# Kernel optimization log

Measured on AMD Instinct MI355X. Metric: run time of the kernel, lower is better.

Reference implementation:

```python
import jax, jax.numpy as jnp
import numpy as np

LN_EPS = 1e-5

def _ln(x, g, b):
    m = x.mean(-1, keepdims=True)
    v = jnp.mean((x - m) ** 2, axis=-1, keepdims=True)
    return (x - m) * jax.lax.rsqrt(v + LN_EPS) * g + b


def setup_inputs() -> dict:
    key = jax.random.key(0)
    ks = jax.random.split(key, 8)
    B, S, H = 8, 4096, 2048
    V, L, E = 32, 8, 64   # vocab_size, symbol seq_len, embedding_dim
    sc = 0.02
    d = {}
    d["hidden_states"] = jax.random.normal(ks[0], (B, S, H), jnp.float32)
    # uniform in (0,1) for Gumbel noise: g = -log(-log(u))
    d["gumbel_u"] = jax.random.uniform(ks[1], (B, L, V), jnp.float32, 1e-6, 1.0 - 1e-6)
    d["enc_w1"] = jax.random.normal(ks[2], (256, H), jnp.float32) * sc
    d["enc_b1"] = jnp.zeros((256,), jnp.float32)
    d["ln1_g"] = jnp.ones((256,), jnp.float32)
    d["ln1_b"] = jnp.zeros((256,), jnp.float32)
    d["enc_w2"] = jax.random.normal(ks[3], (L * V, 256), jnp.float32) * sc
    d["enc_b2"] = jnp.zeros((L * V,), jnp.float32)
    d["embed"] = jax.random.normal(ks[4], (V, E), jnp.float32) * sc
    d["dec_w1"] = jax.random.normal(ks[5], (256, L * E), jnp.float32) * sc
    d["dec_b1"] = jnp.zeros((256,), jnp.float32)
    d["ln2_g"] = jnp.ones((256,), jnp.float32)
    d["ln2_b"] = jnp.zeros((256,), jnp.float32)
    d["dec_w2"] = jax.random.normal(ks[6], (H, 256), jnp.float32) * sc
    d["dec_b2"] = jnp.zeros((H,), jnp.float32)
    return d


def reference(hidden_states, gumbel_u, enc_w1, enc_b1, ln1_g, ln1_b, enc_w2, enc_b2,
              embed, dec_w1, dec_b1, ln2_g, ln2_b, dec_w2, dec_b2):
    V, L, TAU = 32, 8, 1.0
    B, S, H = hidden_states.shape
    E = embed.shape[1]
    # encode: mean-pool over sequence, then MLP -> logits [B, L, V]
    pooled = hidden_states.mean(axis=1)
    h = _ln(pooled @ enc_w1.T + enc_b1, ln1_g, ln1_b)
    h = jax.nn.gelu(h, approximate=False)
    logits = (h @ enc_w2.T + enc_b2).reshape(B, L, V)
    # gumbel-softmax with straight-through (hard) estimator
    g = -jnp.log(-jnp.log(gumbel_u))
    y_soft = jax.nn.softmax((logits + g) / TAU, axis=-1)
    idx = jnp.argmax(y_soft, axis=-1)
    y_hard = jax.nn.one_hot(idx, V, dtype=y_soft.dtype)
    soft_symbols = y_hard - jax.lax.stop_gradient(y_soft) + y_soft
    # decode: embed symbols, flatten, MLP back to hidden size
    emb = jnp.einsum('blv,ve->ble', soft_symbols, embed).reshape(B, L * E)
    dh = _ln(emb @ dec_w1.T + dec_b1, ln2_g, ln2_b)
    dh = jax.nn.gelu(dh, approximate=False)
    decoded = dh @ dec_w2.T + dec_b2            # [B, H]
    # residual + 0.1 * broadcast over sequence
    return hidden_states + 0.1 * decoded[:, None, :]
```

## Files before the change

kernel.cpp:

```cpp
#include <hip/hip_runtime.h>
#include <math.h>

#define B 8
#define S 4096
#define H 2048
#define LSYM 8
#define EMB 64
#define SPLIT 128
#define CHUNK (S / SPLIT)

__global__ __launch_bounds__(256) void pool_partial(const float* __restrict__ hid,
                                                    float* __restrict__ part) {
    const int sp = blockIdx.x;
    const int b  = blockIdx.y;
    const int t  = threadIdx.x;
    const float* slab = hid + (size_t)b * S * H + (size_t)sp * CHUNK * H;
    const int iters = CHUNK * (H / 1024);
    float4 a0 = {0.f, 0.f, 0.f, 0.f};
    float4 a1 = {0.f, 0.f, 0.f, 0.f};
    float4 a2 = {0.f, 0.f, 0.f, 0.f};
    float4 a3 = {0.f, 0.f, 0.f, 0.f};
#pragma unroll 4
    for (int i = 0; i < iters; i += 4) {
        const float4 v0 = *reinterpret_cast<const float4*>(slab + (size_t)i * 1024 + t * 4);
        const float4 v1 = *reinterpret_cast<const float4*>(slab + (size_t)(i + 1) * 1024 + t * 4);
        const float4 v2 = *reinterpret_cast<const float4*>(slab + (size_t)(i + 2) * 1024 + t * 4);
        const float4 v3 = *reinterpret_cast<const float4*>(slab + (size_t)(i + 3) * 1024 + t * 4);
        a0.x += v0.x; a0.y += v0.y; a0.z += v0.z; a0.w += v0.w;
        a1.x += v1.x; a1.y += v1.y; a1.z += v1.z; a1.w += v1.w;
        a2.x += v2.x; a2.y += v2.y; a2.z += v2.z; a2.w += v2.w;
        a3.x += v3.x; a3.y += v3.y; a3.z += v3.z; a3.w += v3.w;
    }
    float4 e, o;
    e.x = a0.x + a2.x; e.y = a0.y + a2.y; e.z = a0.z + a2.z; e.w = a0.w + a2.w;
    o.x = a1.x + a3.x; o.y = a1.y + a3.y; o.z = a1.z + a3.z; o.w = a1.w + a3.w;
    float* dst = part + ((size_t)sp * B + b) * H;
    *reinterpret_cast<float4*>(dst + t * 4)        = e;
    *reinterpret_cast<float4*>(dst + 1024 + t * 4) = o;
}

__global__ __launch_bounds__(256) void pool_reduce(const float* __restrict__ part,
                                                   float* __restrict__ pooled) {
    const int i4 = blockIdx.x * 256 + threadIdx.x;
    if (i4 >= B * H / 4) return;
    float4 acc = {0.f, 0.f, 0.f, 0.f};
    for (int sp = 0; sp < SPLIT; ++sp) {
        const float4 v = *reinterpret_cast<const float4*>(part + (size_t)sp * B * H + (size_t)i4 * 4);
        acc.x += v.x; acc.y += v.y; acc.z += v.z; acc.w += v.w;
    }
    const float inv = 1.0f / (float)S;
    acc.x *= inv; acc.y *= inv; acc.z *= inv; acc.w *= inv;
    *reinterpret_cast<float4*>(pooled + (size_t)i4 * 4) = acc;
}

__global__ __launch_bounds__(256) void enc1_matvec(const float* __restrict__ pooled,
                                                   const float* __restrict__ ew1,
                                                   const float* __restrict__ eb1,
                                                   float* __restrict__ out1) {
    const int wv   = (blockIdx.x * 256 + threadIdx.x) >> 6;
    const int lane = threadIdx.x & 63;
    const int b = wv >> 8, t = wv & 255;
    const float4* wrow = reinterpret_cast<const float4*>(ew1 + (size_t)t * H);
    const float4* prow = reinterpret_cast<const float4*>(pooled + b * H);
    float acc = 0.f;
#pragma unroll
    for (int i = 0; i < 8; ++i) {
        const float4 w = wrow[lane + 64 * i];
        const float4 p = prow[lane + 64 * i];
        acc += w.x * p.x + w.y * p.y + w.z * p.z + w.w * p.w;
    }
    for (int off = 32; off; off >>= 1) acc += __shfl_xor(acc, off, 64);
    if (lane == 0) out1[b * 256 + t] = acc + eb1[t];
}

__device__ __forceinline__ float block_sum256(float x, float* red) {
    const int t = threadIdx.x;
    red[t] = x;
    __syncthreads();
    for (int s = 128; s > 0; s >>= 1) {
        if (t < s) red[t] += red[t + s];
        __syncthreads();
    }
    const float r = red[0];
    __syncthreads();
    return r;
}

__global__ __launch_bounds__(256) void mlp_middle(
    const float* __restrict__ out1, const float* __restrict__ gu,
    const float* __restrict__ g1,  const float* __restrict__ bb1,
    const float* __restrict__ ew2, const float* __restrict__ eb2,
    const float* __restrict__ emb_tab,
    const float* __restrict__ dw1, const float* __restrict__ db1,
    const float* __restrict__ g2,  const float* __restrict__ bb2,
    float* __restrict__ hs2) {
    __shared__ float red[256];
    __shared__ float hs[256];
    __shared__ float es[LSYM * EMB];

    const int b = blockIdx.x;
    const int t = threadIdx.x;

    float acc = out1[b * 256 + t];
    {
        const float m = block_sum256(acc, red) * (1.0f / 256.0f);
        const float d = acc - m;
        const float v = block_sum256(d * d, red) * (1.0f / 256.0f);
        float x = d * rsqrtf(v + 1e-5f) * g1[t] + bb1[t];
        x = 0.5f * x * (1.0f + erff(x * 0.70710678118654752f));
        hs[t] = x;
    }
    __syncthreads();

    float z;
    {
        float a2 = eb2[t];
        const float* w2row = ew2 + t * 256;
        for (int k = 0; k < 256; k += 4) {
            const float4 w = *reinterpret_cast<const float4*>(w2row + k);
            a2 += w.x * hs[k] + w.y * hs[k + 1] + w.z * hs[k + 2] + w.w * hs[k + 3];
        }
        const float u = gu[b * 256 + t];
        z = a2 - logf(-logf(u));
    }

    {
        int   bi = t & 31;
        float bz = z;
        for (int off = 16; off; off >>= 1) {
            const float oz = __shfl_xor(bz, off, 32);
            const int   oi = __shfl_xor(bi, off, 32);
            if (oz > bz || (oz == bz && oi < bi)) { bz = oz; bi = oi; }
        }
        const int l = t >> 5, v32 = t & 31;
        es[l * EMB + v32]      = emb_tab[bi * EMB + v32];
        es[l * EMB + 32 + v32] = emb_tab[bi * EMB + 32 + v32];
    }
    __syncthreads();

    float a3 = db1[t];
    {
        const float* d1row = dw1 + t * (LSYM * EMB);
        for (int k = 0; k < LSYM * EMB; k += 4) {
            const float4 w = *reinterpret_cast<const float4*>(d1row + k);
            a3 += w.x * es[k] + w.y * es[k + 1] + w.z * es[k + 2] + w.w * es[k + 3];
        }
    }
    {
        const float m2 = block_sum256(a3, red) * (1.0f / 256.0f);
        const float dd = a3 - m2;
        const float vv = block_sum256(dd * dd, red) * (1.0f / 256.0f);
        float y = dd * rsqrtf(vv + 1e-5f) * g2[t] + bb2[t];
        y = 0.5f * y * (1.0f + erff(y * 0.70710678118654752f));
        hs2[b * 256 + t] = y;
    }
}

__global__ __launch_bounds__(256) void dec2_matvec(const float* __restrict__ hs2,
                                                   const float* __restrict__ dw2,
                                                   const float* __restrict__ db2,
                                                   float* __restrict__ dec_sc) {
    const int wv   = (blockIdx.x * 256 + threadIdx.x) >> 6;
    const int lane = threadIdx.x & 63;
    const int b = wv >> 11, j = wv & 2047;
    const float4 w = reinterpret_cast<const float4*>(dw2 + (size_t)j * 256)[lane];
    const float4 h = reinterpret_cast<const float4*>(hs2 + b * 256)[lane];
    float acc = w.x * h.x + w.y * h.y + w.z * h.z + w.w * h.w;
    for (int off = 32; off; off >>= 1) acc += __shfl_xor(acc, off, 64);
    if (lane == 0) dec_sc[b * 2048 + j] = 0.1f * (acc + db2[j]);
}

__global__ __launch_bounds__(256) void residual_add(const float* __restrict__ hid,
                                                    const float* __restrict__ dec,
                                                    float* __restrict__ out) {
    const size_t tid0 = (size_t)blockIdx.x * 256 + threadIdx.x;
    const int h4 = (int)(tid0 & (H / 4 - 1));
    const float4* __restrict__ hv4 = reinterpret_cast<const float4*>(hid);
    const float4* __restrict__ dv4 = reinterpret_cast<const float4*>(dec);
    float4* __restrict__ ov4 = reinterpret_cast<float4*>(out);
    size_t i = tid0;
#pragma unroll
    for (int b = 0; b < B; ++b) {
        const float4 dv = dv4[b * (H / 4) + h4];
#pragma unroll
        for (int r = 0; r < 4; ++r, i += (size_t)1 << 19) {
            const float4 hv = hv4[i];
            float4 o;
            o.x = hv.x + dv.x; o.y = hv.y + dv.y; o.z = hv.z + dv.z; o.w = hv.w + dv.w;
            ov4[i] = o;
        }
    }
}

extern "C" void kernel_launch(void* const* d_in, const int* in_sizes, int n_in,
                              void* d_out, int out_size, void* d_ws, size_t ws_size,
                              hipStream_t stream) {
    const float* hid   = (const float*)d_in[0];
    const float* gu    = (const float*)d_in[1];
    const float* ew1   = (const float*)d_in[2];
    const float* eb1   = (const float*)d_in[3];
    const float* g1    = (const float*)d_in[4];
    const float* bb1   = (const float*)d_in[5];
    const float* ew2   = (const float*)d_in[6];
    const float* eb2   = (const float*)d_in[7];
    const float* emb   = (const float*)d_in[8];
    const float* dw1   = (const float*)d_in[9];
    const float* db1   = (const float*)d_in[10];
    const float* g2    = (const float*)d_in[11];
    const float* bb2   = (const float*)d_in[12];
    const float* dw2   = (const float*)d_in[13];
    const float* db2   = (const float*)d_in[14];
    float* out = (float*)d_out;

    float* part   = (float*)d_ws;
    float* pooled = part + (size_t)SPLIT * B * H;
    float* dec_sc = pooled + (size_t)B * H;
    float* out1   = dec_sc + (size_t)B * H;
    float* hs2    = out1 + (size_t)B * 256;

    pool_partial<<<dim3(SPLIT, B), 256, 0, stream>>>(hid, part);
    pool_reduce<<<(B * H / 4 + 255) / 256, 256, 0, stream>>>(part, pooled);
    enc1_matvec<<<B * 256 / 4, 256, 0, stream>>>(pooled, ew1, eb1, out1);
    mlp_middle<<<B, 256, 0, stream>>>(out1, gu, g1, bb1, ew2, eb2, emb,
                                      dw1, db1, g2, bb2, hs2);
    dec2_matvec<<<B * 2048 / 4, 256, 0, stream>>>(hs2, dw2, db2, dec_sc);
    residual_add<<<2048, 256, 0, stream>>>(hid, dec_sc, out);
}
```

Before: 211.3 us.

## Fuse pool reduce, encoder MLP, gumbel and decoder into one kernel

Merges pool_reduce, enc1_matvec, mlp_middle and dec2_matvec into a single 1024-thread kernel with 4 blocks per batch. Each block redundantly recomputes the pooled vector and encoder/decoder MLP, then computes one quarter of the dec_w2 outputs. It also halves SPLIT and widens the pool_partial unroll to 8 accumulators. This removes three launches and several global round-trips, but it runs the small-MLP stage on only 32 blocks and duplicates work across them, which may leave the serial middle section slower.

```diff
diff --git a/kernel.cpp b/kernel.cpp
--- a/kernel.cpp
+++ b/kernel.cpp
@@ -6,8 +6,9 @@
 #define H 2048
 #define LSYM 8
 #define EMB 64
-#define SPLIT 128
+#define SPLIT 64
 #define CHUNK (S / SPLIT)
+#define QPB 4
 
 __global__ __launch_bounds__(256) void pool_partial(const float* __restrict__ hid,
                                                     float* __restrict__ part) {
@@ -16,115 +17,111 @@
     const int t  = threadIdx.x;
     const float* slab = hid + (size_t)b * S * H + (size_t)sp * CHUNK * H;
     const int iters = CHUNK * (H / 1024);
-    float4 a0 = {0.f, 0.f, 0.f, 0.f};
-    float4 a1 = {0.f, 0.f, 0.f, 0.f};
-    float4 a2 = {0.f, 0.f, 0.f, 0.f};
-    float4 a3 = {0.f, 0.f, 0.f, 0.f};
-#pragma unroll 4
-    for (int i = 0; i < iters; i += 4) {
-        const float4 v0 = *reinterpret_cast<const float4*>(slab + (size_t)i * 1024 + t * 4);
-        const float4 v1 = *reinterpret_cast<const float4*>(slab + (size_t)(i + 1) * 1024 + t * 4);
-        const float4 v2 = *reinterpret_cast<const float4*>(slab + (size_t)(i + 2) * 1024 + t * 4);
-        const float4 v3 = *reinterpret_cast<const float4*>(slab + (size_t)(i + 3) * 1024 + t * 4);
-        a0.x += v0.x; a0.y += v0.y; a0.z += v0.z; a0.w += v0.w;
-        a1.x += v1.x; a1.y += v1.y; a1.z += v1.z; a1.w += v1.w;
-        a2.x += v2.x; a2.y += v2.y; a2.z += v2.z; a2.w += v2.w;
-        a3.x += v3.x; a3.y += v3.y; a3.z += v3.z; a3.w += v3.w;
+    float4 a[8];
+#pragma unroll
+    for (int k = 0; k < 8; ++k) a[k] = make_float4(0.f, 0.f, 0.f, 0.f);
+    for (int i = 0; i < iters; i += 8) {
+#pragma unroll
+        for (int k = 0; k < 8; ++k) {
+            const float4 v = *reinterpret_cast<const float4*>(slab + (size_t)(i + k) * 1024 + t * 4);
+            a[k].x += v.x; a[k].y += v.y; a[k].z += v.z; a[k].w += v.w;
+        }
     }
     float4 e, o;
-    e.x = a0.x + a2.x; e.y = a0.y + a2.y; e.z = a0.z + a2.z; e.w = a0.w + a2.w;
-    o.x = a1.x + a3.x; o.y = a1.y + a3.y; o.z = a1.z + a3.z; o.w = a1.w + a3.w;
+    e.x = a[0].x + a[2].x + a[4].x + a[6].x;  e.y = a[0].y + a[2].y + a[4].y + a[6].y;
+    e.z = a[0].z + a[2].z + a[4].z + a[6].z;  e.w = a[0].w + a[2].w + a[4].w + a[6].w;
+    o.x = a[1].x + a[3].x + a[5].x + a[7].x;  o.y = a[1].y + a[3].y + a[5].y + a[7].y;
+    o.z = a[1].z + a[3].z + a[5].z + a[7].z;  o.w = a[1].w + a[3].w + a[5].w + a[7].w;
     float* dst = part + ((size_t)sp * B + b) * H;
     *reinterpret_cast<float4*>(dst + t * 4)        = e;
     *reinterpret_cast<float4*>(dst + 1024 + t * 4) = o;
 }
 
-__global__ __launch_bounds__(256) void pool_reduce(const float* __restrict__ part,
-                                                   float* __restrict__ pooled) {
-    const int i4 = blockIdx.x * 256 + threadIdx.x;
-    if (i4 >= B * H / 4) return;
-    float4 acc = {0.f, 0.f, 0.f, 0.f};
-    for (int sp = 0; sp < SPLIT; ++sp) {
-        const float4 v = *reinterpret_cast<const float4*>(part + (size_t)sp * B * H + (size_t)i4 * 4);
-        acc.x += v.x; acc.y += v.y; acc.z += v.z; acc.w += v.w;
-    }
-    const float inv = 1.0f / (float)S;
-    acc.x *= inv; acc.y *= inv; acc.z *= inv; acc.w *= inv;
-    *reinterpret_cast<float4*>(pooled + (size_t)i4 * 4) = acc;
-}
-
-__global__ __launch_bounds__(256) void enc1_matvec(const float* __restrict__ pooled,
-                                                   const float* __restrict__ ew1,
-                                                   const float* __restrict__ eb1,
-                                                   float* __restrict__ out1) {
-    const int wv   = (blockIdx.x * 256 + threadIdx.x) >> 6;
-    const int lane = threadIdx.x & 63;
-    const int b = wv >> 8, t = wv & 255;
-    const float4* wrow = reinterpret_cast<const float4*>(ew1 + (size_t)t * H);
-    const float4* prow = reinterpret_cast<const float4*>(pooled + b * H);
-    float acc = 0.f;
-#pragma unroll
-    for (int i = 0; i < 8; ++i) {
-        const float4 w = wrow[lane + 64 * i];
-        const float4 p = prow[lane + 64 * i];
-        acc += w.x * p.x + w.y * p.y + w.z * p.z + w.w * p.w;
-    }
-    for (int off = 32; off; off >>= 1) acc += __shfl_xor(acc, off, 64);
-    if (lane == 0) out1[b * 256 + t] = acc + eb1[t];
-}
-
-__device__ __forceinline__ float block_sum256(float x, float* red) {
+__device__ __forceinline__ float block_sum1024(float x, float* red16) {
     const int t = threadIdx.x;
-    red[t] = x;
-    __syncthreads();
-    for (int s = 128; s > 0; s >>= 1) {
-        if (t < s) red[t] += red[t + s];
-        __syncthreads();
-    }
-    const float r = red[0];
+    const int lane = t & 63, wv = t >> 6;
+    for (int off = 32; off; off >>= 1) x += __shfl_xor(x, off, 64);
+    if (lane == 0) red16[wv] = x;
+    __syncthreads();
+    float r = 0.f;
+#pragma unroll
+    for (int i = 0; i < 16; ++i) r += red16[i];
     __syncthreads();
     return r;
 }
 
-__global__ __launch_bounds__(256) void mlp_middle(
-    const float* __restrict__ out1, const float* __restrict__ gu,
+__global__ __launch_bounds__(1024) void mega(
+    const float* __restrict__ part, const float* __restrict__ gu,
+    const float* __restrict__ ew1, const float* __restrict__ eb1,
     const float* __restrict__ g1,  const float* __restrict__ bb1,
     const float* __restrict__ ew2, const float* __restrict__ eb2,
     const float* __restrict__ emb_tab,
     const float* __restrict__ dw1, const float* __restrict__ db1,
     const float* __restrict__ g2,  const float* __restrict__ bb2,
-    float* __restrict__ hs2) {
-    __shared__ float red[256];
-    __shared__ float hs[256];
+    const float* __restrict__ dw2, const float* __restrict__ db2,
+    float* __restrict__ dec_sc) {
+    __shared__ float pooled[H];
+    __shared__ float red16[16];
+    __shared__ float out1s[256];
+    __shared__ float hsm[256];
     __shared__ float es[LSYM * EMB];
-
-    const int b = blockIdx.x;
+    __shared__ float hs2s[256];
+
+    const int blk = blockIdx.x;
+    const int b = blk >> 2, q = blk & (QPB - 1);
     const int t = threadIdx.x;
-
-    float acc = out1[b * 256 + t];
-    {
-        const float m = block_sum256(acc, red) * (1.0f / 256.0f);
-        const float d = acc - m;
-        const float v = block_sum256(d * d, red) * (1.0f / 256.0f);
-        float x = d * rsqrtf(v + 1e-5f) * g1[t] + bb1[t];
+    const int wv = t >> 6, lane = t & 63;
+
+    if (t < H / 4) {
+        const float4* pp = reinterpret_cast<const float4*>(part);
+        float4 acc = {0.f, 0.f, 0.f, 0.f};
+#pragma unroll 4
+        for (int sp = 0; sp < SPLIT; ++sp) {
+            const float4 v = pp[((size_t)sp * B + b) * (H / 4) + t];
+            acc.x += v.x; acc.y += v.y; acc.z += v.z; acc.w += v.w;
+        }
+        const float inv = 1.0f / (float)S;
+        acc.x *= inv; acc.y *= inv; acc.z *= inv; acc.w *= inv;
+        *reinterpret_cast<float4*>(&pooled[t * 4]) = acc;
+    }
+    __syncthreads();
+
+#pragma unroll
+    for (int k = 0; k < 16; ++k) {
+        const int tt = wv * 16 + k;
+        const float4* wrow = reinterpret_cast<const float4*>(ew1 + (size_t)tt * H);
+        float acc = 0.f;
+#pragma unroll
+        for (int i = 0; i < 8; ++i) {
+            const float4 w = wrow[lane + 64 * i];
+            const float4 p = *reinterpret_cast<const float4*>(&pooled[(lane + 64 * i) * 4]);
+            acc += w.x * p.x + w.y * p.y + w.z * p.z + w.w * p.w;
+        }
+        for (int off = 32; off; off >>= 1) acc += __shfl_xor(acc, off, 64);
+        if (lane == 0) out1s[tt] = acc + eb1[tt];
+    }
+    __syncthreads();
+
+    float x0 = (t < 256) ? out1s[t] : 0.f;
+    const float m1 = block_sum1024(x0, red16) * (1.0f / 256.0f);
+    const float d1 = (t < 256) ? (x0 - m1) : 0.f;
+    const float v1 = block_sum1024(d1 * d1, red16) * (1.0f / 256.0f);
+    if (t < 256) {
+        float x = d1 * rsqrtf(v1 + 1e-5f) * g1[t] + bb1[t];
         x = 0.5f * x * (1.0f + erff(x * 0.70710678118654752f));
-        hs[t] = x;
-    }
-    __syncthreads();
-
-    float z;
-    {
+        hsm[t] = x;
+    }
+    __syncthreads();
+
+    if (t < 256) {
         float a2 = eb2[t];
         const float* w2row = ew2 + t * 256;
         for (int k = 0; k < 256; k += 4) {
             const float4 w = *reinterpret_cast<const float4*>(w2row + k);
-            a2 += w.x * hs[k] + w.y * hs[k + 1] + w.z * hs[k + 2] + w.w * hs[k + 3];
+            a2 += w.x * hsm[k] + w.y * hsm[k + 1] + w.z * hsm[k + 2] + w.w * hsm[k + 3];
         }
         const float u = gu[b * 256 + t];
-        z = a2 - logf(-logf(u));
-    }
-
-    {
+        const float z = a2 - logf(-logf(u));
         int   bi = t & 31;
         float bz = z;
         for (int off = 16; off; off >>= 1) {
@@ -138,36 +135,34 @@
     }
     __syncthreads();
 
-    float a3 = db1[t];
-    {
+    float a3 = 0.f;
+    if (t < 256) {
+        a3 = db1[t];
         const float* d1row = dw1 + t * (LSYM * EMB);
         for (int k = 0; k < LSYM * EMB; k += 4) {
             const float4 w = *reinterpret_cast<const float4*>(d1row + k);
             a3 += w.x * es[k] + w.y * es[k + 1] + w.z * es[k + 2] + w.w * es[k + 3];
         }
     }
-    {
-        const float m2 = block_sum256(a3, red) * (1.0f / 256.0f);
-        const float dd = a3 - m2;
-        const float vv = block_sum256(dd * dd, red) * (1.0f / 256.0f);
-        float y = dd * rsqrtf(vv + 1e-5f) * g2[t] + bb2[t];
+    const float m2 = block_sum1024((t < 256) ? a3 : 0.f, red16) * (1.0f / 256.0f);
+    const float d2 = (t < 256) ? (a3 - m2) : 0.f;
+    const float v2 = block_sum1024(d2 * d2, red16) * (1.0f / 256.0f);
+    if (t < 256) {
+        float y = d2 * rsqrtf(v2 + 1e-5f) * g2[t] + bb2[t];
         y = 0.5f * y * (1.0f + erff(y * 0.70710678118654752f));
-        hs2[b * 256 + t] = y;
-    }
-}
-
-__global__ __launch_bounds__(256) void dec2_matvec(const float* __restrict__ hs2,
-                                                   const float* __restrict__ dw2,
-                                                   const float* __restrict__ db2,
-                                                   float* __restrict__ dec_sc) {
-    const int wv   = (blockIdx.x * 256 + threadIdx.x) >> 6;
-    const int lane = threadIdx.x & 63;
-    const int b = wv >> 11, j = wv & 2047;
-    const float4 w = reinterpret_cast<const float4*>(dw2 + (size_t)j * 256)[lane];
-    const float4 h = reinterpret_cast<const float4*>(hs2 + b * 256)[lane];
-    float acc = w.x * h.x + w.y * h.y + w.z * h.z + w.w * h.w;
-    for (int off = 32; off; off >>= 1) acc += __shfl_xor(acc, off, 64);
-    if (lane == 0) dec_sc[b * 2048 + j] = 0.1f * (acc + db2[j]);
+        hs2s[t] = y;
+    }
+    __syncthreads();
+
+    const float4 hvec = *reinterpret_cast<const float4*>(&hs2s[lane * 4]);
+#pragma unroll
+    for (int k = 0; k < 32; ++k) {
+        const int j = q * 512 + wv * 32 + k;
+        const float4 w = reinterpret_cast<const float4*>(dw2 + (size_t)j * 256)[lane];
+        float acc = w.x * hvec.x + w.y * hvec.y + w.z * hvec.z + w.w * hvec.w;
+        for (int off = 32; off; off >>= 1) acc += __shfl_xor(acc, off, 64);
+        if (lane == 0) dec_sc[b * 2048 + j] = 0.1f * (acc + db2[j]);
+    }
 }
 
 __global__ __launch_bounds__(256) void residual_add(const float* __restrict__ hid,
@@ -213,16 +208,10 @@
     float* out = (float*)d_out;
 
     float* part   = (float*)d_ws;
-    float* pooled = part + (size_t)SPLIT * B * H;
-    float* dec_sc = pooled + (size_t)B * H;
-    float* out1   = dec_sc + (size_t)B * H;
-    float* hs2    = out1 + (size_t)B * 256;
+    float* dec_sc = part + (size_t)SPLIT * B * H;
 
     pool_partial<<<dim3(SPLIT, B), 256, 0, stream>>>(hid, part);
-    pool_reduce<<<(B * H / 4 + 255) / 256, 256, 0, stream>>>(part, pooled);
-    enc1_matvec<<<B * 256 / 4, 256, 0, stream>>>(pooled, ew1, eb1, out1);
-    mlp_middle<<<B, 256, 0, stream>>>(out1, gu, g1, bb1, ew2, eb2, emb,
-                                      dw1, db1, g2, bb2, hs2);
-    dec2_matvec<<<B * 2048 / 4, 256, 0, stream>>>(hs2, dw2, db2, dec_sc);
+    mega<<<B * QPB, 1024, 0, stream>>>(part, gu, ew1, eb1, g1, bb1, ew2, eb2, emb,
+                                       dw1, db1, g2, bb2, dw2, db2, dec_sc);
     residual_add<<<2048, 256, 0, stream>>>(hid, dec_sc, out);
 }
```

Measured after the change: 250.8 us. +18.7%, slower.
